# Kernel optimization log

Measured on AMD Instinct MI355X. Metric: run time of the kernel, lower is better.

The kernel has to match this reference:

```python
import jax, jax.numpy as jnp
import numpy as np

N_QUBITS = 12
BATCH = 2048
N_CLASSES = 10


def build_tape(n):
    # 2 layers of: RX on all wires (id 0), RY (id 1), RZ (id 2), then a CRX ring
    # (id 4 forward in layer 0, id 5 reversed in layer 1). 96 gates total for n=12.
    tape = []
    for layer in range(2):
        for i in range(n):
            tape.append(("rx", (i,)))
        for i in range(n):
            tape.append(("ry", (i,)))
        for i in range(n):
            tape.append(("rz", (i,)))
        order = range(n) if layer == 0 else range(n - 1, -1, -1)
        for i in order:
            tape.append(("crx", (i, (i + 1) % n)))
    return tape


def rx_mat(t):
    c = jnp.cos(t / 2).astype(jnp.complex64)
    s = jnp.sin(t / 2).astype(jnp.complex64)
    return jnp.stack([jnp.stack([c, -1j * s]), jnp.stack([-1j * s, c])])


def ry_mat(t):
    c = jnp.cos(t / 2).astype(jnp.complex64)
    s = jnp.sin(t / 2).astype(jnp.complex64)
    return jnp.stack([jnp.stack([c, -s]), jnp.stack([s, c])])


def rz_mat(t):
    em = jnp.exp(-1j * t.astype(jnp.complex64) / 2)
    ep = jnp.exp(1j * t.astype(jnp.complex64) / 2)
    z = jnp.zeros((), jnp.complex64)
    return jnp.stack([jnp.stack([em, z]), jnp.stack([z, ep])])


def apply_1q(psi, U, w):
    # psi: [B] + [2]*n, gate on wire w (axis 1+w)
    psi = jnp.moveaxis(psi, 1 + w, -1)
    psi = psi @ U.T
    return jnp.moveaxis(psi, -1, 1 + w)


def apply_crx(psi, theta, c, t):
    a_c, a_t = 1 + c, 1 + t
    psi = jnp.moveaxis(psi, a_c, 1)  # control -> axis 1
    if a_t < a_c:
        a_t += 1
    psi = jnp.moveaxis(psi, a_t, -1)  # target -> last axis
    U = rx_mat(theta)
    p1 = psi[:, 1] @ U.T  # apply RX only on control=1 branch
    psi = jnp.stack([psi[:, 0], p1], axis=1)
    psi = jnp.moveaxis(psi, -1, a_t)
    return jnp.moveaxis(psi, 1, a_c)


def expvals(psi, n):
    # <X_i>, <Y_i>, <Z_i> for each qubit; returns [B, 3n] ordered X..Y..Z (PL order)
    xs, ys, zs = [], [], []
    for i in range(n):
        p = jnp.moveaxis(psi, 1 + i, -1).reshape(psi.shape[0], -1, 2)
        z = jnp.sum(jnp.abs(p[..., 0]) ** 2 - jnp.abs(p[..., 1]) ** 2, axis=1)
        cross = jnp.sum(jnp.conj(p[..., 0]) * p[..., 1], axis=1)
        xs.append(2.0 * jnp.real(cross))
        ys.append(2.0 * jnp.imag(cross))
        zs.append(jnp.real(z))
    return jnp.stack(xs + ys + zs, axis=1).astype(jnp.float32)


def setup_inputs() -> dict:
    key = jax.random.key(0)
    k0, k1, k2 = jax.random.split(key, 3)
    sv = jax.random.normal(k0, (BATCH, 2 ** N_QUBITS), dtype=jnp.float32)
    sv = sv / jnp.linalg.norm(sv, axis=1, keepdims=True)  # valid quantum states
    n_gates = len(build_tape(N_QUBITS))
    angles = jax.random.normal(k1, (n_gates,), dtype=jnp.float32)
    W = jax.random.normal(k2, (N_CLASSES, 3 * N_QUBITS), dtype=jnp.float32) * 0.1
    b = jnp.zeros((N_CLASSES,), jnp.float32)
    return {"state_vectors": sv, "angles": angles, "W": W, "b": b}


def reference(state_vectors, angles, W, b):
    tape = build_tape(N_QUBITS)
    psi = state_vectors.astype(jnp.complex64).reshape((-1,) + (2,) * N_QUBITS)
    for g, (kind, wires) in enumerate(tape):
        th = angles[g]
        if kind == "rx":
            psi = apply_1q(psi, rx_mat(th), wires[0])
        elif kind == "ry":
            psi = apply_1q(psi, ry_mat(th), wires[0])
        elif kind == "rz":
            psi = apply_1q(psi, rz_mat(th), wires[0])
        else:
            psi = apply_crx(psi, th, wires[0], wires[1])
    feats = expvals(psi, N_QUBITS)  # [B, 3*n_qubits]
    return feats @ W.T + b
```

## Files before the change

### kernel.cpp

```cpp
#include <hip/hip_runtime.h>

#define DIM 4096
using F2 = float2;


__device__ __forceinline__ int caddrA (int r, int t) { return ((r >> 1) << 7) | t; }
__device__ __forceinline__ int caddrB1(int r, int t) { return ((t >> 3) << 7) | ((r >> 1) << 3) | (t & 7); }
__device__ __forceinline__ int caddrB2(int r, int t) { return ((t >> 3) << 7) | ((r & 1) << 6) | ((r >> 2) << 3) | (t & 7); }
__device__ __forceinline__ int caddrC2(int r, int t) { return ((r & 1) << 10) | (t << 3) | (r >> 2); }
__device__ __forceinline__ int s1(int a) { return a ^ ((a >> 5) & 8); }
__device__ __forceinline__ int s2(int a) { return a ^ ((a >> 4) & 15); }

__device__ __forceinline__ F2 pk_mul_bl(F2 a, F2 u) {
    F2 d;
    asm("v_pk_mul_f32 %0, %1, %2 op_sel:[0,0] op_sel_hi:[1,0]"
        : "=v"(d) : "v"(a), "v"(u));
    return d;
}
__device__ __forceinline__ void pk_cross(F2& d, F2 a, F2 u) {
    asm("v_pk_fma_f32 %0, %1, %2, %0 op_sel:[1,1,0] op_sel_hi:[0,1,1] neg_lo:[1,0,0]"
        : "+v"(d) : "v"(a), "v"(u));
}
__device__ __forceinline__ void pk_fma_bl(F2& d, F2 a, F2 u) {
    asm("v_pk_fma_f32 %0, %1, %2, %0 op_sel:[0,0,0] op_sel_hi:[1,0,1]"
        : "+v"(d) : "v"(a), "v"(u));
}
__device__ __forceinline__ void pk_swapneg(F2& d, F2 a, F2 cs) {
    asm("v_pk_fma_f32 %0, %1, %2, %0 op_sel:[1,1,0] op_sel_hi:[0,1,1] neg_hi:[1,0,0]"
        : "+v"(d) : "v"(a), "v"(cs));
}
__device__ __forceinline__ void pk_fma(F2& d, F2 a, F2 b) {
    asm("v_pk_fma_f32 %0, %1, %2, %0" : "+v"(d) : "v"(a), "v"(b));
}
__device__ __forceinline__ void pk_imacc(F2& d, F2 a0, F2 a1) {
    asm("v_pk_fma_f32 %0, %1, %2, %0 op_sel:[0,1,0] op_sel_hi:[1,0,1] neg_hi:[1,0,0]"
        : "+v"(d) : "v"(a0), "v"(a1));
}
__device__ __forceinline__ F2 pk_cmul(F2 u, F2 a) {
    F2 d = pk_mul_bl(a, u);
    pk_cross(d, a, u);
    return d;
}
__device__ __forceinline__ void pk_cfma(F2& d, F2 u, F2 a) {
    pk_fma_bl(d, a, u);
    pk_cross(d, a, u);
}

__device__ __forceinline__ void build_u(float tx, float ty, float tz, float* u) {
    float sx = sinf(0.5f*tx), cx = cosf(0.5f*tx);
    float sy = sinf(0.5f*ty), cy = cosf(0.5f*ty);
    float sz = sinf(0.5f*tz), cz = cosf(0.5f*tz);
    float A00r = cy*cx, A00i =  sy*sx;
    float A01r = -sy*cx, A01i = -cy*sx;
    float A10r =  sy*cx, A10i = -cy*sx;
    float A11r =  cy*cx, A11i = -sy*sx;
    u[0] = cz*A00r + sz*A00i;  u[1] = cz*A00i - sz*A00r;
    u[2] = cz*A01r + sz*A01i;  u[3] = cz*A01i - sz*A01r;
    u[4] = cz*A10r - sz*A10i;  u[5] = cz*A10i + sz*A10r;
    u[6] = cz*A11r - sz*A11i;  u[7] = cz*A11i + sz*A11r;
}

__global__ void prep_kernel(const float* __restrict__ ang, float* __restrict__ coef) {
    int t = threadIdx.x;
    if (t < 12) {
        float u[8]; build_u(ang[t], ang[12+t], ang[24+t], u);
#pragma unroll
        for (int j = 0; j < 8; ++j) coef[t*8 + j] = u[j];
    } else if (t < 24) {
        int q = t - 12;
        float u[8]; build_u(ang[48+q], ang[60+q], ang[72+q], u);
#pragma unroll
        for (int j = 0; j < 8; ++j) coef[192 + q*8 + j] = u[j];
    } else if (t < 36) {
        int c = t - 24;
        float th = 0.5f * ang[95 - c];
        coef[296 + c*2]     = cosf(th);
        coef[296 + c*2 + 1] = sinf(th);
    } else if (t < 47) {
        int q = t - 35;
        float u[8]; build_u(ang[q], ang[12+q], ang[24+q], u);
        float c = cosf(0.5f*ang[36+q-1]), s = sinf(0.5f*ang[36+q-1]);
        float m[8];
        m[0] = c*u[0] + s*u[5];  m[1] = c*u[1] - s*u[4];
        m[2] = c*u[2] + s*u[7];  m[3] = c*u[3] - s*u[6];
        m[4] = s*u[1] + c*u[4];  m[5] = -s*u[0] + c*u[5];
        m[6] = s*u[3] + c*u[6];  m[7] = -s*u[2] + c*u[7];
#pragma unroll
        for (int j = 0; j < 8; ++j) coef[96 + q*8 + j] = m[j];
    } else if (t == 47) {
        float u[8]; build_u(ang[48], ang[60], ang[72], u);
        float c = cosf(0.5f*ang[47]), s = sinf(0.5f*ang[47]);
        float m[8];
        m[0] = c*u[0] + s*u[3];  m[1] = c*u[1] - s*u[2];
        m[2] = s*u[1] + c*u[2];  m[3] = -s*u[0] + c*u[3];
        m[4] = c*u[4] + s*u[7];  m[5] = c*u[5] - s*u[6];
        m[6] = s*u[5] + c*u[6];  m[7] = -s*u[4] + c*u[7];
#pragma unroll
        for (int j = 0; j < 8; ++j) coef[288 + j] = m[j];
    }
}

template<int M, int SB, int HB>
__device__ __forceinline__ void g1q(F2* amp, const float* __restrict__ u) {
    F2 u00 = {u[0], u[1]}, u01 = {u[2], u[3]};
    F2 u10 = {u[4], u[5]}, u11 = {u[6], u[7]};
#pragma unroll
    for (int r0 = 0; r0 < 32; ++r0) {
        if (r0 & M) continue;
        if (SB != 0 && (r0 & SB) != HB) continue;
        const int r1 = r0 + M;
        F2 a0 = amp[r0], a1 = amp[r1];
        F2 n0 = pk_cmul(u00, a0); pk_cfma(n0, u01, a1);
        F2 n1 = pk_cmul(u10, a0); pk_cfma(n1, u11, a1);
        amp[r0] = n0; amp[r1] = n1;
    }
}

template<int MSEL, int M, int SB, int HB>
__device__ __forceinline__ void fg1q(F2* amp, const float* __restrict__ uA,
                                     const float* __restrict__ uB) {
    F2 a00 = {uA[0], uA[1]}, a01 = {uA[2], uA[3]}, a10 = {uA[4], uA[5]}, a11 = {uA[6], uA[7]};
    F2 b00 = {uB[0], uB[1]}, b01 = {uB[2], uB[3]}, b10 = {uB[4], uB[5]}, b11 = {uB[6], uB[7]};
#pragma unroll
    for (int r0 = 0; r0 < 32; ++r0) {
        if (r0 & M) continue;
        if (SB != 0 && (r0 & SB) != HB) continue;
        const int r1 = r0 + M;
        const bool sel = (r0 & MSEL) != 0;
        F2 u00 = sel ? b00 : a00, u01 = sel ? b01 : a01;
        F2 u10 = sel ? b10 : a10, u11 = sel ? b11 : a11;
        F2 a0 = amp[r0], a1 = amp[r1];
        F2 n0 = pk_cmul(u00, a0); pk_cfma(n0, u01, a1);
        F2 n1 = pk_cmul(u10, a0); pk_cfma(n1, u11, a1);
        amp[r0] = n0; amp[r1] = n1;
    }
}

template<int MC, int MT>
__device__ __forceinline__ void crx(F2* amp, F2 cs) {
#pragma unroll
    for (int r0 = 0; r0 < 32; ++r0) {
        if (!(r0 & MC) || (r0 & MT)) continue;
        const int r1 = r0 + MT;
        F2 a0 = amp[r0], a1 = amp[r1];
        F2 n0 = pk_mul_bl(a0, cs); pk_swapneg(n0, a1, cs);
        F2 n1 = pk_mul_bl(a1, cs); pk_swapneg(n1, a0, cs);
        amp[r0] = n0; amp[r1] = n1;
    }
}

template<int M>
__device__ __forceinline__ void expv(const F2* amp, int q, int lane,
                                     float& fx, float& fy, float& fz) {
    F2 zp = {0.f, 0.f}, zm = {0.f, 0.f}, xp = {0.f, 0.f}, ip = {0.f, 0.f};
#pragma unroll
    for (int r0 = 0; r0 < 32; ++r0) {
        if (r0 & M) continue;
        const int r1 = r0 + M;
        F2 a0 = amp[r0], a1 = amp[r1];
        pk_fma(zp, a0, a0);
        pk_fma(zm, a1, a1);
        pk_fma(xp, a0, a1);
        pk_imacc(ip, a0, a1);
    }
    float zz = (zp.x + zp.y) - (zm.x + zm.y);
    float xr = 2.f * (xp.x + xp.y);
    float xi = 2.f * (ip.x + ip.y);
#pragma unroll
    for (int off = 32; off; off >>= 1) {
        xr += __shfl_xor(xr, off);
        xi += __shfl_xor(xi, off);
        zz += __shfl_xor(zz, off);
    }
    if (lane == q) { fx = xr; fy = xi; fz = zz; }
}

template<int M, int SB>
__device__ __forceinline__ int r0_of(int j, int hb) {
    int r = hb ? SB : 0, b = 1;
#pragma unroll
    for (int p = 0; p < 5; ++p) {
        const int mm = 1 << p;
        if (mm == M || mm == SB) continue;
        if (j & b) r |= mm;
        b <<= 1;
    }
    return r;
}

#define ST_H(CADDR, SWZ, SB, HB) \
  { _Pragma("unroll") for (int r = 0; r < 32; ++r) { \
      if ((r & (SB)) != (HB)) continue; \
      psi[SWZ(CADDR(r, t))] = amp[r]; } }
#define LD_H(CADDR, SWZ, M, SB, HB) \
  { _Pragma("unroll") for (int k = 0; k < 16; ++k) { \
      const int j = k >> 1; \
      const int r0 = r0_of<M, SB>(j, (HB) != 0); \
      const int r = (k & 1) ? (r0 + (M)) : r0; \
      amp[r] = psi[SWZ(CADDR(r, t))]; } }

#define U0P(q, M)               g1q<M, 0, 0>(amp, cf + (q)*8)
#define FU0(q, MS, M)           fg1q<MS, M, 0, 0>(amp, cf + (q)*8, cf + 96 + (q)*8)
#define FU0_H(q, MS, M, SB, HB) fg1q<MS, M, SB, HB>(amp, cf + (q)*8, cf + 96 + (q)*8)
#define U1P(q, M)               g1q<M, 0, 0>(amp, cf + 192 + (q)*8)
#define U1P_H(q, M, SB, HB)     g1q<M, SB, HB>(amp, cf + 192 + (q)*8)
#define FU1_0()                 fg1q<4, 1, 0, 0>(amp, cf + 192, cf + 288)
#define CR1(c, MC, MT)          crx<MC, MT>(amp, F2{cf[296 + (c)*2], cf[296 + (c)*2 + 1]})
#define EXPV(q, M)              expv<M>(amp, q, lane, fx, fy, fz)

__global__ __launch_bounds__(128, 1)
void qsim_kernel(const float* __restrict__ sv,
                 const float* __restrict__ cf,
                 const float* __restrict__ W,
                 const float* __restrict__ bvec,
                 float* __restrict__ out)
{
    __shared__ F2 psi[2048];
    const int t = threadIdx.x;
    const int b = blockIdx.x;
    const int lane = t & 63, w = t >> 6;

    F2 amp[32];
    const float* svb = sv + (size_t)b * DIM;
#pragma unroll
    for (int r = 0; r < 32; ++r)
        amp[r] = make_float2(svb[(r << 7) | t], 0.f);

    float fx = 0.f, fy = 0.f, fz = 0.f;

    U0P(0, 16);
    FU0(1, 16, 8); FU0(2, 8, 4); FU0(3, 4, 2); FU0(4, 2, 1);

    ST_H(caddrA, s1, 1, 0);
    __syncthreads();
    LD_H(caddrB1, s1, 16, 1, 0);
    __syncthreads();
    ST_H(caddrA, s1, 1, 1);
    FU0_H(5, 1, 16, 1, 0);
    __syncthreads();
    LD_H(caddrB1, s1, 16, 1, 1);
    FU0_H(5, 1, 16, 1, 1);

    FU0(6, 16, 8); FU0(7, 8, 4); FU0(8, 4, 2);

    __syncthreads();
    ST_H(caddrB2, s2, 2, 0);
    __syncthreads();
    LD_H(caddrC2, s2, 16, 2, 0);
    __syncthreads();
    ST_H(caddrB2, s2, 2, 2);
    FU0_H(9, 2, 16, 2, 0);
    __syncthreads();
    LD_H(caddrC2, s2, 16, 2, 2);
    FU0_H(9, 2, 16, 2, 2);

    FU0(10, 16, 8); FU0(11, 8, 4);
    FU1_0();
    U1P(8, 2); U1P(9, 16); U1P(10, 8); U1P(11, 4);
    CR1(11, 4, 1); CR1(10, 8, 4); CR1(9, 16, 8); CR1(8, 2, 16);

    __syncthreads();
    ST_H(caddrC2, s2, 2, 0);
    EXPV(9, 16); EXPV(10, 8); EXPV(11, 4);
    __syncthreads();
    LD_H(caddrB2, s2, 1, 2, 0);
    __syncthreads();
    ST_H(caddrC2, s2, 2, 2);
    U1P_H(4, 1, 2, 0);
    __syncthreads();
    LD_H(caddrB2, s2, 1, 2, 2);
    U1P_H(4, 1, 2, 2);

    U1P(5, 16); U1P(6, 8); U1P(7, 4);
    CR1(7, 4, 2); CR1(6, 8, 4); CR1(5, 16, 8); CR1(4, 1, 16);

    __syncthreads();
    ST_H(caddrB1, s1, 1, 0);
    EXPV(5, 16); EXPV(6, 8); EXPV(7, 4); EXPV(8, 2);
    __syncthreads();
    LD_H(caddrA, s1, 8, 1, 0);
    __syncthreads();
    ST_H(caddrB1, s1, 1, 1);
    U1P_H(1, 8, 1, 0);
    __syncthreads();
    LD_H(caddrA, s1, 8, 1, 1);
    U1P_H(1, 8, 1, 1);

    U1P(2, 4); U1P(3, 2);
    CR1(3, 2, 1); CR1(2, 4, 2); CR1(1, 8, 4); CR1(0, 16, 8);
    EXPV(0, 16); EXPV(1, 8); EXPV(2, 4); EXPV(3, 2); EXPV(4, 1);

    __syncthreads();
    float* fbuf = (float*)psi;
    if (lane < 12) {
        fbuf[w * 36 + lane]      = fx;
        fbuf[w * 36 + 12 + lane] = fy;
        fbuf[w * 36 + 24 + lane] = fz;
    }
    __syncthreads();
    if (t < 10) {
        float a = bvec[t];
#pragma unroll
        for (int f = 0; f < 36; ++f)
            a += W[t * 36 + f] * (fbuf[f] + fbuf[36 + f]);
        out[(size_t)b * 10 + t] = a;
    }
}

extern "C" void kernel_launch(void* const* d_in, const int* in_sizes, int n_in,
                              void* d_out, int out_size, void* d_ws, size_t ws_size,
                              hipStream_t stream) {
    const float* sv     = (const float*)d_in[0];
    const float* angles = (const float*)d_in[1];
    const float* W      = (const float*)d_in[2];
    const float* bvec   = (const float*)d_in[3];
    float* out  = (float*)d_out;
    float* coef = (float*)d_ws;
    int batch = in_sizes[0] / DIM;
    prep_kernel<<<1, 64, 0, stream>>>(angles, coef);
    qsim_kernel<<<batch, 128, 0, stream>>>(sv, coef, W, bvec, out);
}
```

Baseline: 133.2 us.

## Use one wavefront per state with 64 register amplitudes per thread

```diff
diff --git a/kernel.cpp b/kernel.cpp
--- a/kernel.cpp
+++ b/kernel.cpp
@@ -4,12 +4,17 @@
 using F2 = float2;
 
 
-__device__ __forceinline__ int caddrA (int r, int t) { return ((r >> 1) << 7) | t; }
-__device__ __forceinline__ int caddrB1(int r, int t) { return ((t >> 3) << 7) | ((r >> 1) << 3) | (t & 7); }
-__device__ __forceinline__ int caddrB2(int r, int t) { return ((t >> 3) << 7) | ((r & 1) << 6) | ((r >> 2) << 3) | (t & 7); }
-__device__ __forceinline__ int caddrC2(int r, int t) { return ((r & 1) << 10) | (t << 3) | (r >> 2); }
-__device__ __forceinline__ int s1(int a) { return a ^ ((a >> 5) & 8); }
-__device__ __forceinline__ int s2(int a) { return a ^ ((a >> 4) & 15); }
+__device__ __forceinline__ int caddrA (int r, int t) { return ((r >> 1) << 6) | t; }
+__device__ __forceinline__ int caddrB1(int r, int t) { return ((t >> 1) << 6) | (r & 62) | (t & 1); }
+__device__ __forceinline__ int caddrB2(int r, int t) {
+    return ((t >> 1) << 6) | ((r & 1) << 5) | (((r >> 4) & 3) << 3)
+         | (((r >> 1) & 3) << 1) | (t & 1);
+}
+__device__ __forceinline__ int caddrC2(int r, int t) {
+    return (((r >> 1) & 1) << 10) | ((r & 1) << 9) | (t << 3)
+         | (((r >> 5) & 1) << 2) | (((r >> 4) & 1) << 1) | ((r >> 2) & 1);
+}
+__device__ __forceinline__ int swz(int a) { return a ^ ((a >> 6) & 15); }
 
 __device__ __forceinline__ F2 pk_mul_bl(F2 a, F2 u) {
     F2 d;
@@ -105,7 +110,7 @@
     F2 u00 = {u[0], u[1]}, u01 = {u[2], u[3]};
     F2 u10 = {u[4], u[5]}, u11 = {u[6], u[7]};
 #pragma unroll
-    for (int r0 = 0; r0 < 32; ++r0) {
+    for (int r0 = 0; r0 < 64; ++r0) {
         if (r0 & M) continue;
         if (SB != 0 && (r0 & SB) != HB) continue;
         const int r1 = r0 + M;
@@ -122,7 +127,7 @@
     F2 a00 = {uA[0], uA[1]}, a01 = {uA[2], uA[3]}, a10 = {uA[4], uA[5]}, a11 = {uA[6], uA[7]};
     F2 b00 = {uB[0], uB[1]}, b01 = {uB[2], uB[3]}, b10 = {uB[4], uB[5]}, b11 = {uB[6], uB[7]};
 #pragma unroll
-    for (int r0 = 0; r0 < 32; ++r0) {
+    for (int r0 = 0; r0 < 64; ++r0) {
         if (r0 & M) continue;
         if (SB != 0 && (r0 & SB) != HB) continue;
         const int r1 = r0 + M;
@@ -139,7 +144,7 @@
 template<int MC, int MT>
 __device__ __forceinline__ void crx(F2* amp, F2 cs) {
 #pragma unroll
-    for (int r0 = 0; r0 < 32; ++r0) {
+    for (int r0 = 0; r0 < 64; ++r0) {
         if (!(r0 & MC) || (r0 & MT)) continue;
         const int r1 = r0 + MT;
         F2 a0 = amp[r0], a1 = amp[r1];
@@ -154,7 +159,7 @@
                                      float& fx, float& fy, float& fz) {
     F2 zp = {0.f, 0.f}, zm = {0.f, 0.f}, xp = {0.f, 0.f}, ip = {0.f, 0.f};
 #pragma unroll
-    for (int r0 = 0; r0 < 32; ++r0) {
+    for (int r0 = 0; r0 < 64; ++r0) {
         if (r0 & M) continue;
         const int r1 = r0 + M;
         F2 a0 = amp[r0], a1 = amp[r1];
@@ -179,7 +184,7 @@
 __device__ __forceinline__ int r0_of(int j, int hb) {
     int r = hb ? SB : 0, b = 1;
 #pragma unroll
-    for (int p = 0; p < 5; ++p) {
+    for (int p = 0; p < 6; ++p) {
         const int mm = 1 << p;
         if (mm == M || mm == SB) continue;
         if (j & b) r |= mm;
@@ -188,27 +193,27 @@
     return r;
 }
 
-#define ST_H(CADDR, SWZ, SB, HB) \
-  { _Pragma("unroll") for (int r = 0; r < 32; ++r) { \
+#define ST_H(CADDR, SB, HB) \
+  { _Pragma("unroll") for (int r = 0; r < 64; ++r) { \
       if ((r & (SB)) != (HB)) continue; \
-      psi[SWZ(CADDR(r, t))] = amp[r]; } }
-#define LD_H(CADDR, SWZ, M, SB, HB) \
-  { _Pragma("unroll") for (int k = 0; k < 16; ++k) { \
+      psi[swz(CADDR(r, t))] = amp[r]; } }
+#define LD_H(CADDR, M, SB, HB) \
+  { _Pragma("unroll") for (int k = 0; k < 32; ++k) { \
       const int j = k >> 1; \
       const int r0 = r0_of<M, SB>(j, (HB) != 0); \
       const int r = (k & 1) ? (r0 + (M)) : r0; \
-      amp[r] = psi[SWZ(CADDR(r, t))]; } }
+      amp[r] = psi[swz(CADDR(r, t))]; } }
 
 #define U0P(q, M)               g1q<M, 0, 0>(amp, cf + (q)*8)
 #define FU0(q, MS, M)           fg1q<MS, M, 0, 0>(amp, cf + (q)*8, cf + 96 + (q)*8)
 #define FU0_H(q, MS, M, SB, HB) fg1q<MS, M, SB, HB>(amp, cf + (q)*8, cf + 96 + (q)*8)
 #define U1P(q, M)               g1q<M, 0, 0>(amp, cf + 192 + (q)*8)
 #define U1P_H(q, M, SB, HB)     g1q<M, SB, HB>(amp, cf + 192 + (q)*8)
-#define FU1_0()                 fg1q<4, 1, 0, 0>(amp, cf + 192, cf + 288)
+#define FU1_0()                 fg1q<4, 2, 0, 0>(amp, cf + 192, cf + 288)
 #define CR1(c, MC, MT)          crx<MC, MT>(amp, F2{cf[296 + (c)*2], cf[296 + (c)*2 + 1]})
-#define EXPV(q, M)              expv<M>(amp, q, lane, fx, fy, fz)
-
-__global__ __launch_bounds__(128, 1)
+#define EXPV(q, M)              expv<M>(amp, q, t, fx, fy, fz)
+
+__global__ __launch_bounds__(64, 1)
 void qsim_kernel(const float* __restrict__ sv,
                  const float* __restrict__ cf,
                  const float* __restrict__ W,
@@ -218,91 +223,91 @@
     __shared__ F2 psi[2048];
     const int t = threadIdx.x;
     const int b = blockIdx.x;
-    const int lane = t & 63, w = t >> 6;
-
-    F2 amp[32];
+
+    F2 amp[64];
     const float* svb = sv + (size_t)b * DIM;
 #pragma unroll
-    for (int r = 0; r < 32; ++r)
-        amp[r] = make_float2(svb[(r << 7) | t], 0.f);
+    for (int k = 0; k < 64; ++k) {
+        const int r = (k & 1) ? ((k >> 1) + 32) : (k >> 1);
+        amp[r] = make_float2(svb[(r << 6) | t], 0.f);
+    }
 
     float fx = 0.f, fy = 0.f, fz = 0.f;
 
-    U0P(0, 16);
-    FU0(1, 16, 8); FU0(2, 8, 4); FU0(3, 4, 2); FU0(4, 2, 1);
-
-    ST_H(caddrA, s1, 1, 0);
-    __syncthreads();
-    LD_H(caddrB1, s1, 16, 1, 0);
-    __syncthreads();
-    ST_H(caddrA, s1, 1, 1);
-    FU0_H(5, 1, 16, 1, 0);
-    __syncthreads();
-    LD_H(caddrB1, s1, 16, 1, 1);
-    FU0_H(5, 1, 16, 1, 1);
-
-    FU0(6, 16, 8); FU0(7, 8, 4); FU0(8, 4, 2);
-
-    __syncthreads();
-    ST_H(caddrB2, s2, 2, 0);
-    __syncthreads();
-    LD_H(caddrC2, s2, 16, 2, 0);
-    __syncthreads();
-    ST_H(caddrB2, s2, 2, 2);
-    FU0_H(9, 2, 16, 2, 0);
-    __syncthreads();
-    LD_H(caddrC2, s2, 16, 2, 2);
-    FU0_H(9, 2, 16, 2, 2);
-
-    FU0(10, 16, 8); FU0(11, 8, 4);
+    U0P(0, 32);
+    FU0(1, 32, 16); FU0(2, 16, 8); FU0(3, 8, 4); FU0(4, 4, 2); FU0(5, 2, 1);
+
+    ST_H(caddrA, 1, 0);
+    __syncthreads();
+    LD_H(caddrB1, 32, 1, 0);
+    __syncthreads();
+    ST_H(caddrA, 1, 1);
+    FU0_H(6, 1, 32, 1, 0);
+    __syncthreads();
+    LD_H(caddrB1, 32, 1, 1);
+    FU0_H(6, 1, 32, 1, 1);
+
+    FU0(7, 32, 16); FU0(8, 16, 8); FU0(9, 8, 4); FU0(10, 4, 2);
+
+    __syncthreads();
+    ST_H(caddrB2, 8, 0);
+    __syncthreads();
+    LD_H(caddrC2, 4, 8, 0);
+    __syncthreads();
+    ST_H(caddrB2, 8, 8);
+    FU0_H(11, 16, 4, 8, 0);
+    __syncthreads();
+    LD_H(caddrC2, 4, 8, 8);
+    FU0_H(11, 16, 4, 8, 8);
+
     FU1_0();
-    U1P(8, 2); U1P(9, 16); U1P(10, 8); U1P(11, 4);
-    CR1(11, 4, 1); CR1(10, 8, 4); CR1(9, 16, 8); CR1(8, 2, 16);
-
-    __syncthreads();
-    ST_H(caddrC2, s2, 2, 0);
-    EXPV(9, 16); EXPV(10, 8); EXPV(11, 4);
-    __syncthreads();
-    LD_H(caddrB2, s2, 1, 2, 0);
-    __syncthreads();
-    ST_H(caddrC2, s2, 2, 2);
-    U1P_H(4, 1, 2, 0);
-    __syncthreads();
-    LD_H(caddrB2, s2, 1, 2, 2);
-    U1P_H(4, 1, 2, 2);
-
-    U1P(5, 16); U1P(6, 8); U1P(7, 4);
-    CR1(7, 4, 2); CR1(6, 8, 4); CR1(5, 16, 8); CR1(4, 1, 16);
-
-    __syncthreads();
-    ST_H(caddrB1, s1, 1, 0);
-    EXPV(5, 16); EXPV(6, 8); EXPV(7, 4); EXPV(8, 2);
-    __syncthreads();
-    LD_H(caddrA, s1, 8, 1, 0);
-    __syncthreads();
-    ST_H(caddrB1, s1, 1, 1);
-    U1P_H(1, 8, 1, 0);
-    __syncthreads();
-    LD_H(caddrA, s1, 8, 1, 1);
-    U1P_H(1, 8, 1, 1);
-
-    U1P(2, 4); U1P(3, 2);
-    CR1(3, 2, 1); CR1(2, 4, 2); CR1(1, 8, 4); CR1(0, 16, 8);
-    EXPV(0, 16); EXPV(1, 8); EXPV(2, 4); EXPV(3, 2); EXPV(4, 1);
+    U1P(1, 1); U1P(8, 8); U1P(9, 32); U1P(10, 16); U1P(11, 4);
+    CR1(11, 4, 2); CR1(10, 16, 4); CR1(9, 32, 16); CR1(8, 8, 32);
+
+    __syncthreads();
+    ST_H(caddrC2, 8, 0);
+    EXPV(9, 32); EXPV(10, 16); EXPV(11, 4);
+    __syncthreads();
+    LD_H(caddrB2, 1, 8, 0);
+    __syncthreads();
+    ST_H(caddrC2, 8, 8);
+    U1P_H(5, 1, 8, 0);
+    __syncthreads();
+    LD_H(caddrB2, 1, 8, 8);
+    U1P_H(5, 1, 8, 8);
+
+    U1P(6, 32); U1P(7, 16);
+    CR1(7, 16, 8); CR1(6, 32, 16); CR1(5, 1, 32);
+
+    __syncthreads();
+    ST_H(caddrB1, 1, 0);
+    EXPV(6, 32); EXPV(7, 16); EXPV(8, 8);
+    __syncthreads();
+    LD_H(caddrA, 8, 1, 0);
+    __syncthreads();
+    ST_H(caddrB1, 1, 1);
+    U1P_H(2, 8, 1, 0);
+    __syncthreads();
+    LD_H(caddrA, 8, 1, 1);
+    U1P_H(2, 8, 1, 1);
+
+    U1P(3, 4); U1P(4, 2);
+    CR1(4, 2, 1); CR1(3, 4, 2); CR1(2, 8, 4); CR1(1, 16, 8); CR1(0, 32, 16);
+    EXPV(0, 32); EXPV(1, 16); EXPV(2, 8); EXPV(3, 4); EXPV(4, 2); EXPV(5, 1);
 
     __syncthreads();
     float* fbuf = (float*)psi;
-    if (lane < 12) {
-        fbuf[w * 36 + lane]      = fx;
-        fbuf[w * 36 + 12 + lane] = fy;
-        fbuf[w * 36 + 24 + lane] = fz;
+    if (t < 12) {
+        fbuf[t]      = fx;
+        fbuf[12 + t] = fy;
+        fbuf[24 + t] = fz;
     }
     __syncthreads();
     if (t < 10) {
         float a = bvec[t];
 #pragma unroll
         for (int f = 0; f < 36; ++f)
-            a += W[t * 36 + f] * (fbuf[f] + fbuf[36 + f]);
+            a += W[t * 36 + f] * fbuf[f];
         out[(size_t)b * 10 + t] = a;
     }
 }
@@ -318,5 +323,5 @@
     float* coef = (float*)d_ws;
     int batch = in_sizes[0] / DIM;
     prep_kernel<<<1, 64, 0, stream>>>(angles, coef);
-    qsim_kernel<<<batch, 128, 0, stream>>>(sv, coef, W, bvec, out);
-}
+    qsim_kernel<<<batch, 64, 0, stream>>>(sv, coef, W, bvec, out);
+}
```

Measured after the change: 148.6 us. 11.5% more time.
